# Kernel tuning notes

Hardware: AMD Instinct MI355X
Metric: run time of the kernel (lower is better)

The kernel has to match this reference:

```python
import jax, jax.numpy as jnp
import numpy as np

TOP_K = 8
NUM_GROUPS = 8


def setup_inputs() -> dict:
    key = jax.random.key(0)
    ks = jax.random.split(key, 6)
    T_B, T_S, H, I, E, G = 1, 2048, 2048, 768, 32, NUM_GROUPS
    hidden_states = jax.random.normal(ks[0], (T_B, T_S, H), dtype=jnp.float32)
    gate_weight = jax.random.normal(ks[1], (E, H), dtype=jnp.float32) * 0.02
    gate_up_proj = jax.random.normal(ks[2], (E, 2 * I, H), dtype=jnp.float32) * 0.02
    down_proj = jax.random.normal(ks[3], (E, H, I), dtype=jnp.float32) * 0.02
    merge_groups = jax.random.randint(ks[4], (E,), 0, G, dtype=jnp.int64)
    # ensure every group id appears at least once so dominant experts are well-defined
    merge_groups = merge_groups.at[:G].set(jnp.arange(G, dtype=jnp.int64))
    dominant_experts = jax.random.randint(ks[5], (G,), 0, E, dtype=jnp.int64)
    return {
        "hidden_states": hidden_states,
        "gate_weight": gate_weight,
        "gate_up_proj": gate_up_proj,
        "down_proj": down_proj,
        "merge_groups": merge_groups,
        "dominant_experts": dominant_experts,
    }


def reference(hidden_states, gate_weight, gate_up_proj, down_proj, merge_groups, dominant_experts):
    B, S, H = hidden_states.shape
    G = dominant_experts.shape[0]
    x = hidden_states.reshape(-1, H)  # [T, H]

    # Router: softmax over all experts, then top-k of the probabilities (as in source)
    logits = jnp.einsum("th,eh->te", x, gate_weight)
    probs = jax.nn.softmax(logits.astype(jnp.float32), axis=-1).astype(logits.dtype)
    top_val, top_idx = jax.lax.top_k(probs, TOP_K)  # [T, K]
    top_val = top_val / jnp.sum(top_val, axis=-1, keepdims=True)  # norm_topk_prob

    # Each selected expert e is replaced by its group's dominant expert; by linearity
    # of the scatter-add combine, sum routing weights per (token, group).
    sel_group = merge_groups[top_idx]  # [T, K] in [0, G)
    onehot = jax.nn.one_hot(sel_group, G, dtype=top_val.dtype)  # [T, K, G]
    w_tg = jnp.einsum("tk,tkg->tg", top_val, onehot)  # combined weight per token/group

    gu = gate_up_proj[dominant_experts]  # [G, 2I, H]
    dn = down_proj[dominant_experts]     # [G, H, I]

    h = jnp.einsum("th,goh->tgo", x, gu)           # [T, G, 2I]
    gate, up = jnp.split(h, 2, axis=-1)              # [T, G, I] each
    act = jax.nn.silu(gate) * up                     # SwiGLU
    y = jnp.einsum("tgi,ghi->tgh", act, dn)        # [T, G, H]
    out = jnp.einsum("tg,tgh->th", w_tg, y)        # combine
    return out.reshape(B, S, H)
```

## Files before the change

kernel.cpp:

```cpp
#include <hip/hip_runtime.h>
#include <hip/hip_bf16.h>

typedef __attribute__((ext_vector_type(8))) short short8v;
typedef __attribute__((ext_vector_type(4))) float f32x4;

#define T_TOK 2048
#define HDIM  2048
#define IDIM  768
#define NGRP  8

__device__ __forceinline__ unsigned short f2b(float f){
  unsigned u = __float_as_uint(f);
  u = u + 0x7FFFu + ((u >> 16) & 1u);
  return (unsigned short)(u >> 16);
}
__device__ __forceinline__ float b2f(unsigned short s){
  return __uint_as_float(((unsigned)s) << 16);
}

__global__ __launch_bounds__(256) void router_kernel(
    const float* __restrict__ x, const float* __restrict__ gw,
    const int* __restrict__ mg, float* __restrict__ wtg,
    unsigned short* __restrict__ xb)
{
  __shared__ float xs[4][2048];
  __shared__ float lg[4][32];
  int tid = threadIdx.x;
  int t0 = blockIdx.x * 4;

  #pragma unroll
  for (int k = 0; k < 8; k++){
    int idx = k*256 + tid;
    int tok = idx >> 9, wi = idx & 511;
    float4 v = ((const float4*)(x + (size_t)(t0 + tok)*HDIM))[wi];
    ((float4*)xs[tok])[wi] = v;
    ushort4 b; b.x=f2b(v.x); b.y=f2b(v.y); b.z=f2b(v.z); b.w=f2b(v.w);
    ((ushort4*)(xb + (size_t)(t0+tok)*HDIM))[wi] = b;
  }
  __syncthreads();

  int e = tid >> 3, ch = tid & 7;
  float s0=0.f, s1=0.f, s2=0.f, s3=0.f;
  const float4* gv = (const float4*)(gw + (size_t)e*HDIM);
  #pragma unroll 4
  for (int k = 0; k < 64; k++){
    int i4 = ch + 8*k;
    float4 b  = gv[i4];
    float4 a0 = ((const float4*)xs[0])[i4];
    float4 a1 = ((const float4*)xs[1])[i4];
    float4 a2 = ((const float4*)xs[2])[i4];
    float4 a3 = ((const float4*)xs[3])[i4];
    s0 += a0.x*b.x + a0.y*b.y + a0.z*b.z + a0.w*b.w;
    s1 += a1.x*b.x + a1.y*b.y + a1.z*b.z + a1.w*b.w;
    s2 += a2.x*b.x + a2.y*b.y + a2.z*b.z + a2.w*b.w;
    s3 += a3.x*b.x + a3.y*b.y + a3.z*b.z + a3.w*b.w;
  }
  #pragma unroll
  for (int off=1; off<8; off<<=1){
    s0 += __shfl_xor(s0, off); s1 += __shfl_xor(s1, off);
    s2 += __shfl_xor(s2, off); s3 += __shfl_xor(s3, off);
  }
  if (ch == 0){ lg[0][e]=s0; lg[1][e]=s1; lg[2][e]=s2; lg[3][e]=s3; }
  __syncthreads();

  int wv = tid >> 6, lane = tid & 63;
  float val = (lane < 32) ? lg[wv][lane] : -1e30f;
  float mx = val;
  #pragma unroll
  for (int off=16; off; off>>=1) mx = fmaxf(mx, __shfl_xor(mx, off));
  float p = (lane < 32) ? expf(val - mx) : 0.f;
  float sm = p;
  #pragma unroll
  for (int off=16; off; off>>=1) sm += __shfl_xor(sm, off);
  float v = (lane < 32) ? (p / sm) : -1.f;
  int idx = lane;
  float vals[8]; int idxs[8];
  #pragma unroll
  for (int it=0; it<8; it++){
    float bv = v; int bi = idx;
    #pragma unroll
    for (int off=32; off; off>>=1){
      float ov = __shfl_xor(bv, off); int oi = __shfl_xor(bi, off);
      if (ov > bv || (ov == bv && oi < bi)){ bv = ov; bi = oi; }
    }
    vals[it] = bv; idxs[it] = bi;
    if (lane == bi) v = -1.f;
  }
  float tot = vals[0]+vals[1]+vals[2]+vals[3]+vals[4]+vals[5]+vals[6]+vals[7];
  float racc = 0.f;
  #pragma unroll
  for (int it=0; it<8; it++){
    int grp = mg[idxs[it]];
    if (lane == grp) racc += vals[it] / tot;
  }
  if (lane < 8) wtg[(size_t)(t0+wv)*NGRP + lane] = racc;
}

__global__ __launch_bounds__(256) void convert_gu_kernel(
    const float* __restrict__ src, unsigned short* __restrict__ dst,
    const int* __restrict__ de)
{
  int g = blockIdx.z;
  int i4 = blockIdx.x*256 + threadIdx.x;
  int j  = i4 >> 9;
  int c4 = i4 & 511;
  int q = j >> 5, r = j & 31;
  int srow = (r < 16) ? (q*16 + r) : (768 + q*16 + (r - 16));
  const float4* s = (const float4*)(src + ((size_t)de[g]*1536 + srow)*HDIM);
  float4 vv = s[c4];
  ushort4 b; b.x=f2b(vv.x); b.y=f2b(vv.y); b.z=f2b(vv.z); b.w=f2b(vv.w);
  ((ushort4*)(dst + ((size_t)g*1536 + j)*HDIM))[c4] = b;
}

__global__ __launch_bounds__(256) void convert_dn_kernel(
    const float* __restrict__ src, unsigned short* __restrict__ dst,
    const int* __restrict__ de)
{
  int g = blockIdx.z;
  size_t i4 = (size_t)blockIdx.x*256 + threadIdx.x;
  const float4* s = (const float4*)(src + (size_t)de[g]*1572864);
  float4 vv = s[i4];
  ushort4 b; b.x=f2b(vv.x); b.y=f2b(vv.y); b.z=f2b(vv.z); b.w=f2b(vv.w);
  ((ushort4*)(dst + (size_t)g*1572864))[i4] = b;
}


__device__ __forceinline__ void stage_half_g(
    const unsigned short* __restrict__ gsrc, int ldElems,
    unsigned short* __restrict__ ldsHalf, int tid)
{
  int rl0 = tid >> 3;
  int cb  = (tid & 7) * 16;
  int w   = tid >> 6;
  #pragma unroll
  for (int j = 0; j < 2; j++){
    int rl  = j*64 + rl0;
    int scb = cb ^ ((rl & 7) << 4);
    const unsigned short* src = gsrc + (size_t)rl*ldElems + (scb >> 1);
    __builtin_amdgcn_global_load_lds(
        (const __attribute__((address_space(1))) void*)src,
        (__attribute__((address_space(3))) void*)(ldsHalf + j*4096 + w*512),
        16, 0, 0);
  }
}

__device__ __forceinline__ void read_b4(const unsigned short* Bb,
                                        short8v (&b)[4][2], int wn, int fr, int colOff)
{
  #pragma unroll
  for (int n=0;n<4;n++){
    const char* rb = (const char*)Bb + (size_t)((wn*64 + n*16 + fr)*128);
    b[n][0] = *(const short8v*)(rb + colOff);
    b[n][1] = *(const short8v*)(rb + (colOff ^ 64));
  }
}

template<int P>
__device__ __forceinline__ void subphase(const unsigned short* Ab, int wm, int fr, int colOff,
                                         const short8v (&b)[4][2], f32x4 (&acc)[8][4])
{
  short8v a[2][2];
  #pragma unroll
  for (int i=0;i<2;i++){
    const char* rb = (const char*)Ab + (size_t)((wm*128 + (P*2+i)*16 + fr)*128);
    a[i][0] = *(const short8v*)(rb + colOff);
    a[i][1] = *(const short8v*)(rb + (colOff ^ 64));
  }
  __builtin_amdgcn_s_setprio(1);
  #pragma unroll
  for (int i=0;i<2;i++){
    #pragma unroll
    for (int n=0;n<4;n++){
      acc[P*2+i][n] = __builtin_amdgcn_mfma_f32_16x16x32_bf16(a[i][0], b[n][0], acc[P*2+i][n],0,0,0);
      acc[P*2+i][n] = __builtin_amdgcn_mfma_f32_16x16x32_bf16(a[i][1], b[n][1], acc[P*2+i][n],0,0,0);
    }
  }
  __builtin_amdgcn_s_setprio(0);
}

#define WAITV(N)  asm volatile("s_waitcnt vmcnt(" #N ")" ::: "memory")

__global__ __launch_bounds__(512, 2) void gemm1_kernel(
    const unsigned short* __restrict__ xb, const unsigned short* __restrict__ gu,
    const float* __restrict__ wtg, unsigned short* __restrict__ actb)
{
  __shared__ unsigned short Al[2][16384];
  __shared__ unsigned short Bl[2][16384];
  int tid = threadIdx.x, lane = tid & 63, w = tid >> 6;
  int wm = w >> 2, wn = w & 3;
  int fr = lane & 15;
  int colOff = ((lane >> 4) * 16) ^ ((fr & 7) << 4);
  int bid = blockIdx.x;
  int P = bid % 48, mb = bid / 48;
  int m0 = mb * 256, n0 = (P % 6) * 256, g = P / 6;
  const unsigned short* Abase = xb + (size_t)m0 * HDIM;
  const unsigned short* Bbase = gu + ((size_t)g * 1536 + n0) * HDIM;

  f32x4 acc[8][4];
  #pragma unroll
  for (int m=0;m<8;m++){
    #pragma unroll
    for (int n=0;n<4;n++) acc[m][n] = (f32x4){0,0,0,0};
  }
  short8v b[4][2];

  #define STG1(buf, kt2) do { \
    stage_half_g(Bbase + (size_t)(kt2)*64,                    HDIM, &Bl[buf][0],    tid); \
    stage_half_g(Bbase + (size_t)128*HDIM + (size_t)(kt2)*64, HDIM, &Bl[buf][8192], tid); \
    stage_half_g(Abase + (size_t)(kt2)*64,                    HDIM, &Al[buf][0],    tid); \
    stage_half_g(Abase + (size_t)128*HDIM + (size_t)(kt2)*64, HDIM, &Al[buf][8192], tid); \
  } while(0)

  STG1(0, 0);
  WAITV(0);
  __builtin_amdgcn_s_barrier();

  for (int kt = 0; kt < 31; ++kt){
    int cur = kt & 1, nb = cur ^ 1;
    STG1(nb, kt+1);
    __builtin_amdgcn_sched_barrier(0);
    read_b4(Bl[cur], b, wn, fr, colOff);
    subphase<0>(Al[cur], wm, fr, colOff, b, acc);
    subphase<1>(Al[cur], wm, fr, colOff, b, acc);
    subphase<2>(Al[cur], wm, fr, colOff, b, acc);
    subphase<3>(Al[cur], wm, fr, colOff, b, acc);
    WAITV(0);
    __builtin_amdgcn_s_barrier();
  }
  read_b4(Bl[1], b, wn, fr, colOff);
  subphase<0>(Al[1], wm, fr, colOff, b, acc);
  subphase<1>(Al[1], wm, fr, colOff, b, acc);
  subphase<2>(Al[1], wm, fr, colOff, b, acc);
  subphase<3>(Al[1], wm, fr, colOff, b, acc);
  #undef STG1

  int r0 = (lane >> 4) * 4;
  int qbase = (n0 + wn * 64) >> 5;
  #pragma unroll
  for (int mi = 0; mi < 8; mi++){
    int trow = m0 + wm*128 + mi*16 + r0;
    #pragma unroll
    for (int q = 0; q < 2; q++){
      int icol = (qbase + q)*16 + fr;
      #pragma unroll
      for (int j = 0; j < 4; j++){
        int t = trow + j;
        float wv = wtg[(size_t)t*NGRP + g];
        float gf = acc[mi][2*q][j];
        float uf = acc[mi][2*q+1][j];
        float sg = gf / (1.f + expf(-gf));
        actb[((size_t)g*T_TOK + t)*IDIM + icol] = f2b(sg * uf * wv);
      }
    }
  }
}

__global__ __launch_bounds__(512, 2) void gemm2_kernel(
    const unsigned short* __restrict__ actb, const unsigned short* __restrict__ dnb,
    float* __restrict__ part)
{
  __shared__ unsigned short Al[2][16384];
  __shared__ unsigned short Bl[2][16384];
  int tid = threadIdx.x, lane = tid & 63, w = tid >> 6;
  int wm = w >> 2, wn = w & 3;
  int fr = lane & 15;
  int colOff = ((lane >> 4) * 16) ^ ((fr & 7) << 4);
  int bid = blockIdx.x;
  int P = bid % 32, mb = bid / 32;
  int m0 = mb * 256, n0 = (P % 8) * 256, z = P / 8;

  f32x4 acc[8][4];
  #pragma unroll
  for (int m=0;m<8;m++){
    #pragma unroll
    for (int n=0;n<4;n++) acc[m][n] = (f32x4){0,0,0,0};
  }
  short8v b[4][2];

  #define STG2(buf, kt2) do { \
    int gi = ((kt2) >= 12) ? 1 : 0; \
    int gg = z*2 + gi; \
    int kk = ((kt2) - gi*12) * 64; \
    const unsigned short* Aseg = actb + (size_t)(gg*T_TOK + m0)*IDIM + kk; \
    const unsigned short* Bseg = dnb  + (size_t)(gg*HDIM + n0)*IDIM + kk; \
    stage_half_g(Bseg,                    IDIM, &Bl[buf][0],    tid); \
    stage_half_g(Bseg + (size_t)128*IDIM, IDIM, &Bl[buf][8192], tid); \
    stage_half_g(Aseg,                    IDIM, &Al[buf][0],    tid); \
    stage_half_g(Aseg + (size_t)128*IDIM, IDIM, &Al[buf][8192], tid); \
  } while(0)

  STG2(0, 0);
  WAITV(0);
  __builtin_amdgcn_s_barrier();

  for (int kt = 0; kt < 23; ++kt){
    int cur = kt & 1, nb = cur ^ 1;
    STG2(nb, kt+1);
    __builtin_amdgcn_sched_barrier(0);
    read_b4(Bl[cur], b, wn, fr, colOff);
    subphase<0>(Al[cur], wm, fr, colOff, b, acc);
    subphase<1>(Al[cur], wm, fr, colOff, b, acc);
    subphase<2>(Al[cur], wm, fr, colOff, b, acc);
    subphase<3>(Al[cur], wm, fr, colOff, b, acc);
    WAITV(0);
    __builtin_amdgcn_s_barrier();
  }
  read_b4(Bl[1], b, wn, fr, colOff);
  subphase<0>(Al[1], wm, fr, colOff, b, acc);
  subphase<1>(Al[1], wm, fr, colOff, b, acc);
  subphase<2>(Al[1], wm, fr, colOff, b, acc);
  subphase<3>(Al[1], wm, fr, colOff, b, acc);
  #undef STG2

  float* Cb = part + (size_t)z * T_TOK * HDIM;
  int r0 = (lane >> 4) * 4;
  #pragma unroll
  for (int mi = 0; mi < 8; mi++){
    int row = m0 + wm*128 + mi*16 + r0;
    #pragma unroll
    for (int n = 0; n < 4; n++){
      int cc = n0 + wn*64 + n*16 + fr;
      #pragma unroll
      for (int j = 0; j < 4; j++){
        Cb[(size_t)(row + j)*HDIM + cc] = acc[mi][n][j];
      }
    }
  }
}

__global__ __launch_bounds__(256) void reduce_kernel(
    const float* __restrict__ p, float* __restrict__ o)
{
  size_t i = ((size_t)blockIdx.x*256 + threadIdx.x)*4;
  float4 a0 = *(const float4*)(p + i);
  float4 a1 = *(const float4*)(p + 4194304 + i);
  float4 a2 = *(const float4*)(p + 8388608 + i);
  float4 a3 = *(const float4*)(p + 12582912 + i);
  float4 r;
  r.x = a0.x + a1.x + a2.x + a3.x;
  r.y = a0.y + a1.y + a2.y + a3.y;
  r.z = a0.z + a1.z + a2.z + a3.z;
  r.w = a0.w + a1.w + a2.w + a3.w;
  *(float4*)(o + i) = r;
}

extern "C" void kernel_launch(void* const* d_in, const int* in_sizes, int n_in,
                              void* d_out, int out_size, void* d_ws, size_t ws_size,
                              hipStream_t stream)
{
  (void)in_sizes; (void)n_in; (void)out_size; (void)ws_size;
  const float* x   = (const float*)d_in[0];
  const float* gw  = (const float*)d_in[1];
  const float* gup = (const float*)d_in[2];
  const float* dnp = (const float*)d_in[3];
  const int*   mg  = (const int*)d_in[4];
  const int*   de  = (const int*)d_in[5];
  float* out = (float*)d_out;
  char* ws = (char*)d_ws;

  float*          wtg  = (float*)(ws + 0);
  unsigned short* xb   = (unsigned short*)(ws + 65536);
  unsigned short* dnb  = (unsigned short*)(ws + 8454144);
  unsigned short* actb = (unsigned short*)(ws + 33619968);
  float*          part = (float*)(ws + 58785792);
  unsigned short* gub  = (unsigned short*)(ws + 58785792);

  router_kernel<<<512, 256, 0, stream>>>(x, gw, mg, wtg, xb);
  convert_gu_kernel<<<dim3(3072,1,8), 256, 0, stream>>>(gup, gub, de);
  convert_dn_kernel<<<dim3(1536,1,8), 256, 0, stream>>>(dnp, dnb, de);
  gemm1_kernel<<<384, 512, 0, stream>>>(xb, gub, wtg, actb);
  gemm2_kernel<<<256, 512, 0, stream>>>(actb, dnb, part);
  reduce_kernel<<<4096, 256, 0, stream>>>(part, out);
}
```

Before: 261.7 us.

## Restructure GEMMs with 4-stage K=32 pipeline, new tiles, XCD-aware block mapping

```diff
diff --git a/kernel.cpp b/kernel.cpp
--- a/kernel.cpp
+++ b/kernel.cpp
@@ -125,129 +125,100 @@
 }
 
 
-__device__ __forceinline__ void stage_half_g(
-    const unsigned short* __restrict__ gsrc, int ldElems,
-    unsigned short* __restrict__ ldsHalf, int tid)
-{
-  int rl0 = tid >> 3;
-  int cb  = (tid & 7) * 16;
-  int w   = tid >> 6;
-  #pragma unroll
-  for (int j = 0; j < 2; j++){
-    int rl  = j*64 + rl0;
-    int scb = cb ^ ((rl & 7) << 4);
-    const unsigned short* src = gsrc + (size_t)rl*ldElems + (scb >> 1);
+template<int R>
+__device__ __forceinline__ void stage_tile(const unsigned short* __restrict__ gsrc,
+                                           int ldE, unsigned short* __restrict__ lds,
+                                           int tid)
+{
+  #pragma unroll
+  for (int j = 0; j < R/128; j++){
+    int row = j*128 + (tid >> 2);
+    const unsigned short* src = gsrc + (size_t)row*ldE + (tid & 3)*8;
     __builtin_amdgcn_global_load_lds(
         (const __attribute__((address_space(1))) void*)src,
-        (__attribute__((address_space(3))) void*)(ldsHalf + j*4096 + w*512),
+        (__attribute__((address_space(3))) void*)(lds + j*4096 + (tid >> 6)*512),
         16, 0, 0);
   }
 }
 
-__device__ __forceinline__ void read_b4(const unsigned short* Bb,
-                                        short8v (&b)[4][2], int wn, int fr, int colOff)
-{
-  #pragma unroll
-  for (int n=0;n<4;n++){
-    const char* rb = (const char*)Bb + (size_t)((wn*64 + n*16 + fr)*128);
-    b[n][0] = *(const short8v*)(rb + colOff);
-    b[n][1] = *(const short8v*)(rb + (colOff ^ 64));
-  }
-}
-
-template<int P>
-__device__ __forceinline__ void subphase(const unsigned short* Ab, int wm, int fr, int colOff,
-                                         const short8v (&b)[4][2], f32x4 (&acc)[8][4])
-{
-  short8v a[2][2];
-  #pragma unroll
-  for (int i=0;i<2;i++){
-    const char* rb = (const char*)Ab + (size_t)((wm*128 + (P*2+i)*16 + fr)*128);
-    a[i][0] = *(const short8v*)(rb + colOff);
-    a[i][1] = *(const short8v*)(rb + (colOff ^ 64));
-  }
-  __builtin_amdgcn_s_setprio(1);
-  #pragma unroll
-  for (int i=0;i<2;i++){
-    #pragma unroll
-    for (int n=0;n<4;n++){
-      acc[P*2+i][n] = __builtin_amdgcn_mfma_f32_16x16x32_bf16(a[i][0], b[n][0], acc[P*2+i][n],0,0,0);
-      acc[P*2+i][n] = __builtin_amdgcn_mfma_f32_16x16x32_bf16(a[i][1], b[n][1], acc[P*2+i][n],0,0,0);
-    }
-  }
-  __builtin_amdgcn_s_setprio(0);
+__device__ __forceinline__ short8v rfrag(const unsigned short* lds, int r, int s){
+  return *(const short8v*)((const char*)lds + r*64 + (s << 4));
 }
 
 #define WAITV(N)  asm volatile("s_waitcnt vmcnt(" #N ")" ::: "memory")
+#define TOPBAR()  do { __builtin_amdgcn_s_barrier(); __builtin_amdgcn_sched_barrier(0); } while(0)
 
 __global__ __launch_bounds__(512, 2) void gemm1_kernel(
     const unsigned short* __restrict__ xb, const unsigned short* __restrict__ gu,
     const float* __restrict__ wtg, unsigned short* __restrict__ actb)
 {
-  __shared__ unsigned short Al[2][16384];
-  __shared__ unsigned short Bl[2][16384];
+  __shared__ unsigned short Al[4][8192];
+  __shared__ unsigned short Bl[4][4096];
   int tid = threadIdx.x, lane = tid & 63, w = tid >> 6;
-  int wm = w >> 2, wn = w & 3;
-  int fr = lane & 15;
-  int colOff = ((lane >> 4) * 16) ^ ((fr & 7) << 4);
+  int wm = w >> 1, wn = w & 1;
+  int fr = lane & 15, sl = lane >> 4;
+
   int bid = blockIdx.x;
-  int P = bid % 48, mb = bid / 48;
-  int m0 = mb * 256, n0 = (P % 6) * 256, g = P / 6;
+  int xcd = bid & 7, j = bid >> 3;
+  int panel = ((xcd & 1) ? 48 : 0) + (j >> 1);
+  int mb = ((xcd >> 1) << 1) + (j & 1);
+  int nb = panel % 12, g = panel / 12;
+  int m0 = mb * 256, n0 = nb * 128;
   const unsigned short* Abase = xb + (size_t)m0 * HDIM;
   const unsigned short* Bbase = gu + ((size_t)g * 1536 + n0) * HDIM;
 
-  f32x4 acc[8][4];
-  #pragma unroll
-  for (int m=0;m<8;m++){
+  f32x4 acc[4][4];
+  #pragma unroll
+  for (int m=0;m<4;m++){
     #pragma unroll
     for (int n=0;n<4;n++) acc[m][n] = (f32x4){0,0,0,0};
   }
-  short8v b[4][2];
-
-  #define STG1(buf, kt2) do { \
-    stage_half_g(Bbase + (size_t)(kt2)*64,                    HDIM, &Bl[buf][0],    tid); \
-    stage_half_g(Bbase + (size_t)128*HDIM + (size_t)(kt2)*64, HDIM, &Bl[buf][8192], tid); \
-    stage_half_g(Abase + (size_t)(kt2)*64,                    HDIM, &Al[buf][0],    tid); \
-    stage_half_g(Abase + (size_t)128*HDIM + (size_t)(kt2)*64, HDIM, &Al[buf][8192], tid); \
+
+  #define BODY1(t, DOSTAGE) do { \
+    int buf = (t) & 3; \
+    short8v av[4], bv[4]; \
+    _Pragma("unroll") for (int m=0;m<4;m++) av[m] = rfrag(&Al[buf][0], wm*64 + m*16 + fr, sl); \
+    _Pragma("unroll") for (int n=0;n<4;n++) bv[n] = rfrag(&Bl[buf][0], wn*64 + n*16 + fr, sl); \
+    if (DOSTAGE){ int k2 = (t)+3, b2 = k2 & 3; \
+      stage_tile<256>(Abase + k2*32, HDIM, &Al[b2][0], tid); \
+      stage_tile<128>(Bbase + k2*32, HDIM, &Bl[b2][0], tid); } \
+    asm volatile("s_waitcnt lgkmcnt(0)" ::: "memory"); \
+    __builtin_amdgcn_sched_barrier(0); \
+    __builtin_amdgcn_s_setprio(1); \
+    _Pragma("unroll") for (int m=0;m<4;m++){ \
+      _Pragma("unroll") for (int n=0;n<4;n++){ \
+        acc[m][n] = __builtin_amdgcn_mfma_f32_16x16x32_bf16(av[m], bv[n], acc[m][n],0,0,0); } } \
+    __builtin_amdgcn_s_setprio(0); \
   } while(0)
 
-  STG1(0, 0);
-  WAITV(0);
-  __builtin_amdgcn_s_barrier();
-
-  for (int kt = 0; kt < 31; ++kt){
-    int cur = kt & 1, nb = cur ^ 1;
-    STG1(nb, kt+1);
-    __builtin_amdgcn_sched_barrier(0);
-    read_b4(Bl[cur], b, wn, fr, colOff);
-    subphase<0>(Al[cur], wm, fr, colOff, b, acc);
-    subphase<1>(Al[cur], wm, fr, colOff, b, acc);
-    subphase<2>(Al[cur], wm, fr, colOff, b, acc);
-    subphase<3>(Al[cur], wm, fr, colOff, b, acc);
-    WAITV(0);
-    __builtin_amdgcn_s_barrier();
-  }
-  read_b4(Bl[1], b, wn, fr, colOff);
-  subphase<0>(Al[1], wm, fr, colOff, b, acc);
-  subphase<1>(Al[1], wm, fr, colOff, b, acc);
-  subphase<2>(Al[1], wm, fr, colOff, b, acc);
-  subphase<3>(Al[1], wm, fr, colOff, b, acc);
-  #undef STG1
+  const int NT = 64;
+  stage_tile<256>(Abase,      HDIM, &Al[0][0], tid); stage_tile<128>(Bbase,      HDIM, &Bl[0][0], tid);
+  stage_tile<256>(Abase + 32, HDIM, &Al[1][0], tid); stage_tile<128>(Bbase + 32, HDIM, &Bl[1][0], tid);
+  stage_tile<256>(Abase + 64, HDIM, &Al[2][0], tid); stage_tile<128>(Bbase + 64, HDIM, &Bl[2][0], tid);
+
+  for (int t = 0; t < NT-3; ++t){
+    WAITV(6); TOPBAR();
+    BODY1(t, 1);
+  }
+  WAITV(6); TOPBAR(); BODY1(NT-3, 0);
+  WAITV(3); TOPBAR(); BODY1(NT-2, 0);
+  WAITV(0); TOPBAR(); BODY1(NT-1, 0);
+  #undef BODY1
 
   int r0 = (lane >> 4) * 4;
-  int qbase = (n0 + wn * 64) >> 5;
-  #pragma unroll
-  for (int mi = 0; mi < 8; mi++){
-    int trow = m0 + wm*128 + mi*16 + r0;
+  int q0 = (n0 + wn*64) >> 5;
+  #pragma unroll
+  for (int m = 0; m < 4; m++){
+    int trow = m0 + wm*64 + m*16 + r0;
     #pragma unroll
     for (int q = 0; q < 2; q++){
-      int icol = (qbase + q)*16 + fr;
+      int icol = (q0 + q)*16 + fr;
       #pragma unroll
-      for (int j = 0; j < 4; j++){
-        int t = trow + j;
+      for (int jj = 0; jj < 4; jj++){
+        int t = trow + jj;
         float wv = wtg[(size_t)t*NGRP + g];
-        float gf = acc[mi][2*q][j];
-        float uf = acc[mi][2*q+1][j];
+        float gf = acc[m][2*q][jj];
+        float uf = acc[m][2*q+1][jj];
         float sg = gf / (1.f + expf(-gf));
         actb[((size_t)g*T_TOK + t)*IDIM + icol] = f2b(sg * uf * wv);
       }
@@ -259,70 +230,71 @@
     const unsigned short* __restrict__ actb, const unsigned short* __restrict__ dnb,
     float* __restrict__ part)
 {
-  __shared__ unsigned short Al[2][16384];
-  __shared__ unsigned short Bl[2][16384];
+  __shared__ unsigned short Al[4][4096];
+  __shared__ unsigned short Bl[4][8192];
   int tid = threadIdx.x, lane = tid & 63, w = tid >> 6;
   int wm = w >> 2, wn = w & 3;
-  int fr = lane & 15;
-  int colOff = ((lane >> 4) * 16) ^ ((fr & 7) << 4);
+  int fr = lane & 15, sl = lane >> 4;
+
   int bid = blockIdx.x;
-  int P = bid % 32, mb = bid / 32;
-  int m0 = mb * 256, n0 = (P % 8) * 256, z = P / 8;
-
-  f32x4 acc[8][4];
-  #pragma unroll
-  for (int m=0;m<8;m++){
+  int xcd = bid & 7, j = bid >> 3;
+  int panel = ((xcd & 1) ? 8 : 0) + (j >> 2);
+  int mb = ((xcd >> 1) << 2) + (j & 3);
+  int nb = panel & 7, z = panel >> 3;
+  int m0 = mb * 128, n0 = nb * 256;
+
+  f32x4 acc[4][4];
+  #pragma unroll
+  for (int m=0;m<4;m++){
     #pragma unroll
     for (int n=0;n<4;n++) acc[m][n] = (f32x4){0,0,0,0};
   }
-  short8v b[4][2];
-
-  #define STG2(buf, kt2) do { \
-    int gi = ((kt2) >= 12) ? 1 : 0; \
-    int gg = z*2 + gi; \
-    int kk = ((kt2) - gi*12) * 64; \
-    const unsigned short* Aseg = actb + (size_t)(gg*T_TOK + m0)*IDIM + kk; \
-    const unsigned short* Bseg = dnb  + (size_t)(gg*HDIM + n0)*IDIM + kk; \
-    stage_half_g(Bseg,                    IDIM, &Bl[buf][0],    tid); \
-    stage_half_g(Bseg + (size_t)128*IDIM, IDIM, &Bl[buf][8192], tid); \
-    stage_half_g(Aseg,                    IDIM, &Al[buf][0],    tid); \
-    stage_half_g(Aseg + (size_t)128*IDIM, IDIM, &Al[buf][8192], tid); \
+
+  #define STAGE2(kt, b2) do { \
+    int gi = (kt) / 24; int kk = ((kt) - gi*24) * 32; int gg = z*4 + gi; \
+    stage_tile<128>(actb + ((size_t)gg*T_TOK + m0)*IDIM + kk, IDIM, &Al[b2][0], tid); \
+    stage_tile<256>(dnb  + ((size_t)gg*HDIM + n0)*IDIM + kk, IDIM, &Bl[b2][0], tid); \
   } while(0)
 
-  STG2(0, 0);
-  WAITV(0);
-  __builtin_amdgcn_s_barrier();
-
-  for (int kt = 0; kt < 23; ++kt){
-    int cur = kt & 1, nb = cur ^ 1;
-    STG2(nb, kt+1);
-    __builtin_amdgcn_sched_barrier(0);
-    read_b4(Bl[cur], b, wn, fr, colOff);
-    subphase<0>(Al[cur], wm, fr, colOff, b, acc);
-    subphase<1>(Al[cur], wm, fr, colOff, b, acc);
-    subphase<2>(Al[cur], wm, fr, colOff, b, acc);
-    subphase<3>(Al[cur], wm, fr, colOff, b, acc);
-    WAITV(0);
-    __builtin_amdgcn_s_barrier();
-  }
-  read_b4(Bl[1], b, wn, fr, colOff);
-  subphase<0>(Al[1], wm, fr, colOff, b, acc);
-  subphase<1>(Al[1], wm, fr, colOff, b, acc);
-  subphase<2>(Al[1], wm, fr, colOff, b, acc);
-  subphase<3>(Al[1], wm, fr, colOff, b, acc);
-  #undef STG2
+  #define BODY2(t, DOSTAGE) do { \
+    int buf = (t) & 3; \
+    short8v av[4], bv[4]; \
+    _Pragma("unroll") for (int m=0;m<4;m++) av[m] = rfrag(&Al[buf][0], wm*64 + m*16 + fr, sl); \
+    _Pragma("unroll") for (int n=0;n<4;n++) bv[n] = rfrag(&Bl[buf][0], wn*64 + n*16 + fr, sl); \
+    if (DOSTAGE){ int k2 = (t)+3; STAGE2(k2, k2 & 3); } \
+    asm volatile("s_waitcnt lgkmcnt(0)" ::: "memory"); \
+    __builtin_amdgcn_sched_barrier(0); \
+    __builtin_amdgcn_s_setprio(1); \
+    _Pragma("unroll") for (int m=0;m<4;m++){ \
+      _Pragma("unroll") for (int n=0;n<4;n++){ \
+        acc[m][n] = __builtin_amdgcn_mfma_f32_16x16x32_bf16(av[m], bv[n], acc[m][n],0,0,0); } } \
+    __builtin_amdgcn_s_setprio(0); \
+  } while(0)
+
+  const int NT = 96;
+  STAGE2(0, 0); STAGE2(1, 1); STAGE2(2, 2);
+
+  for (int t = 0; t < NT-3; ++t){
+    WAITV(6); TOPBAR();
+    BODY2(t, 1);
+  }
+  WAITV(6); TOPBAR(); BODY2(NT-3, 0);
+  WAITV(3); TOPBAR(); BODY2(NT-2, 0);
+  WAITV(0); TOPBAR(); BODY2(NT-1, 0);
+  #undef BODY2
+  #undef STAGE2
 
   float* Cb = part + (size_t)z * T_TOK * HDIM;
   int r0 = (lane >> 4) * 4;
   #pragma unroll
-  for (int mi = 0; mi < 8; mi++){
-    int row = m0 + wm*128 + mi*16 + r0;
+  for (int m = 0; m < 4; m++){
+    int row = m0 + wm*64 + m*16 + r0;
     #pragma unroll
     for (int n = 0; n < 4; n++){
       int cc = n0 + wn*64 + n*16 + fr;
       #pragma unroll
-      for (int j = 0; j < 4; j++){
-        Cb[(size_t)(row + j)*HDIM + cc] = acc[mi][n][j];
+      for (int jj = 0; jj < 4; jj++){
+        Cb[(size_t)(row + jj)*HDIM + cc] = acc[m][n][jj];
       }
     }
   }
@@ -334,13 +306,11 @@
   size_t i = ((size_t)blockIdx.x*256 + threadIdx.x)*4;
   float4 a0 = *(const float4*)(p + i);
   float4 a1 = *(const float4*)(p + 4194304 + i);
-  float4 a2 = *(const float4*)(p + 8388608 + i);
-  float4 a3 = *(const float4*)(p + 12582912 + i);
   float4 r;
-  r.x = a0.x + a1.x + a2.x + a3.x;
-  r.y = a0.y + a1.y + a2.y + a3.y;
-  r.z = a0.z + a1.z + a2.z + a3.z;
-  r.w = a0.w + a1.w + a2.w + a3.w;
+  r.x = a0.x + a1.x;
+  r.y = a0.y + a1.y;
+  r.z = a0.z + a1.z;
+  r.w = a0.w + a1.w;
   *(float4*)(o + i) = r;
 }
 
@@ -362,13 +332,13 @@
   unsigned short* xb   = (unsigned short*)(ws + 65536);
   unsigned short* dnb  = (unsigned short*)(ws + 8454144);
   unsigned short* actb = (unsigned short*)(ws + 33619968);
+  unsigned short* gub  = (unsigned short*)(ws + 58785792);
   float*          part = (float*)(ws + 58785792);
-  unsigned short* gub  = (unsigned short*)(ws + 58785792);
 
   router_kernel<<<512, 256, 0, stream>>>(x, gw, mg, wtg, xb);
   convert_gu_kernel<<<dim3(3072,1,8), 256, 0, stream>>>(gup, gub, de);
   convert_dn_kernel<<<dim3(1536,1,8), 256, 0, stream>>>(dnp, dnb, de);
-  gemm1_kernel<<<384, 512, 0, stream>>>(xb, gub, wtg, actb);
+  gemm1_kernel<<<768, 512, 0, stream>>>(xb, gub, wtg, actb);
   gemm2_kernel<<<256, 512, 0, stream>>>(actb, dnb, part);
   reduce_kernel<<<4096, 256, 0, stream>>>(part, out);
 }
```

Measured after the change: 239.6 us. -8.4%, faster.
